# Kernel optimization log

Hardware: AMD Instinct MI355X
Metric: run time of the kernel (lower is better)

## Reference

```python
import jax, jax.numpy as jnp
import numpy as np

B, N_PTS, M_ROIS = 2, 8192, 2048
C_IN, O, H, NS = 128, 256, 4, 32
RADIUS = 1.6
BN_EPS = 1e-5
SCALE = 10.0  # point cloud extent


def setup_inputs() -> dict:
    key = jax.random.key(0)
    ks = jax.random.split(key, 20)
    f32 = jnp.float32
    Cg = C_IN + 3  # grouper concats relative xyz to features

    def kaiming(k, shape, fan_in):
        return jax.random.normal(k, shape, f32) * np.sqrt(2.0 / fan_in)

    inp = {
        "xyz": jax.random.uniform(ks[0], (B, N_PTS, 3), f32) * SCALE,
        "new_xyz": jax.random.uniform(ks[1], (B, M_ROIS, 3), f32) * SCALE,
        "features": jax.random.normal(ks[2], (B, C_IN, N_PTS), f32),
        # conv1d (kernel=1, no bias) weights, torch layout (out, in)
        "pos_w": kaiming(ks[3], (O, 3), 3),
        "key_w": kaiming(ks[4], (O, Cg), Cg),
        "val_w1": kaiming(ks[5], (O, Cg), Cg),
        "bn1_g": jnp.ones((O,), f32), "bn1_b": jnp.zeros((O,), f32),
        "val_w2": kaiming(ks[6], (O, O), O),
        "bn2_g": jnp.ones((O,), f32), "bn2_b": jnp.zeros((O,), f32),
        "attn_w": kaiming(ks[7], (H, O), O),
        # sigmoid-gated coefficient linears (no bias)
        "kc_w": kaiming(ks[8], (O, O), O),
        "qc_w": kaiming(ks[9], (O, O), O),
        "qkc_w": kaiming(ks[10], (O, O), O),
        "vc_w": kaiming(ks[11], (O, O), O),
        # cls/reg weight MLPs: Linear(O,O//2)+ReLU, Linear(O//2,1)+Sigmoid
        "cls_w1": kaiming(ks[12], (O // 2, O), O), "cls_b1": jnp.zeros((O // 2,), f32),
        "cls_w2": kaiming(ks[13], (1, O // 2), O // 2), "cls_b2": jnp.zeros((1,), f32),
        "reg_w1": kaiming(ks[14], (O // 2, O), O), "reg_b1": jnp.zeros((O // 2,), f32),
        "reg_w2": kaiming(ks[15], (1, O // 2), O // 2), "reg_b2": jnp.zeros((1,), f32),
    }
    return inp


def _bn(x, g, b):
    # eval-mode BatchNorm1d with running_mean=0, running_var=1 (init state)
    return g[None, :, None] * (x * (1.0 / np.sqrt(1.0 + BN_EPS))) + b[None, :, None]


def _conv1x1(w, x):  # (O,C) x (M,C,NS) -> (M,O,NS)
    return jnp.einsum('oc,mcn->mon', w, x)


def _ball_group(pts, q):
    # ball query: first NS points within RADIUS of each query (pad with first hit)
    n_tot = pts.shape[0]
    d2 = jnp.sum((q[:, None, :] - pts[None, :, :]) ** 2, axis=-1)  # (M, Ntot)
    order = jnp.where(d2 < RADIUS ** 2, jnp.arange(n_tot, dtype=jnp.int32), n_tot)
    neg_vals, idx = jax.lax.top_k(-order, NS)  # smallest indices among in-ball pts
    valid = (-neg_vals) < n_tot
    idx = jnp.where(valid, idx, idx[:, :1])  # pad with first neighbor
    has_any = valid[:, :1]
    idx = jnp.where(has_any, idx, 0)  # empty balls -> point 0
    return idx, ~has_any[:, 0]


def reference(xyz, new_xyz, features, pos_w, key_w, val_w1, bn1_g, bn1_b,
              val_w2, bn2_g, bn2_b, attn_w, kc_w, qc_w, qkc_w, vc_w,
              cls_w1, cls_b1, cls_w2, cls_b2, reg_w1, reg_b1, reg_w2, reg_b2):
    pts = xyz.reshape(-1, 3)                                   # (Ntot, 3)
    feats = features.transpose(0, 2, 1).reshape(-1, C_IN)      # (Ntot, C)
    q = new_xyz.reshape(-1, 3)                                 # (M, 3)

    idx, empty_mask = _ball_group(pts, q)                      # (M, NS)
    gx = pts[idx] - q[:, None, :]                              # relative xyz (M,NS,3)
    gxt = gx.transpose(0, 2, 1)                                # (M,3,NS)
    gf = jnp.concatenate([gx, feats[idx]], axis=-1).transpose(0, 2, 1)  # (M,C+3,NS)

    pos = jax.nn.relu(_conv1x1(pos_w, gxt))                    # (M,O,NS)
    key = jax.nn.relu(_conv1x1(key_w, gf))                     # (M,O,NS)
    v = jax.nn.relu(_bn(_conv1x1(val_w1, gf), bn1_g, bn1_b))
    val = jax.nn.relu(_bn(_conv1x1(val_w2, v), bn2_g, bn2_b))  # (M,O,NS)
    pos_key = pos * key

    sig = jax.nn.sigmoid
    v_c = sig(pos.mean(2) @ vc_w.T)                            # (M,O)
    q_c = sig(pos.mean(2) @ qc_w.T)
    k_c = sig(key.mean(2) @ kc_w.T)
    qk_c = sig(pos_key.mean(2) @ qkc_w.T)

    val = val + pos * v_c[:, :, None]
    attn_emb = pos * q_c[:, :, None] + key * k_c[:, :, None] + pos_key * qk_c[:, :, None]
    attn = jax.nn.softmax(jnp.einsum('ho,mon->mhn', attn_w, attn_emb), axis=-1)  # (M,H,NS)

    m = val.shape[0]
    vh = val.reshape(m, H, O // H, NS)
    new_features = jnp.einsum('mhdn,mhn->mhd', vh, attn).reshape(m, O)  # (M,O)

    def gate(x, w1, b1, w2, b2):
        return sig(jax.nn.relu(x @ w1.T + b1) @ w2.T + b2)

    cls_features = new_features * gate(new_features, cls_w1, cls_b1, cls_w2, cls_b2)
    reg_features = new_features * gate(new_features, reg_w1, reg_b1, reg_w2, reg_b2)
    return new_features, cls_features, reg_features
```

## Files before the change

### kernel.cpp

```cpp
#include <hip/hip_runtime.h>

#define DI __device__ __forceinline__

typedef __attribute__((ext_vector_type(8))) short bf16x8;
typedef __attribute__((ext_vector_type(4))) short s16x4;
typedef __attribute__((ext_vector_type(4))) float f32x4;

DI short f2bs(float x){ unsigned u = __float_as_uint(x);
  return (short)((u + 0x7FFF + ((u >> 16) & 1)) >> 16); }
DI float bs2f(short s){ return __uint_as_float(((unsigned)(unsigned short)s) << 16); }
DI f32x4 MFMA(bf16x8 a, bf16x8 b, f32x4 c){
  return __builtin_amdgcn_mfma_f32_16x16x32_bf16(a, b, c, 0, 0, 0);
}

constexpr int NP   = 8192;
constexpr int NTOT = 16384;
constexpr int M    = 4096;
constexpr int C    = 128;
constexpr int O    = 256;
constexpr int NS   = 32;
constexpr int H    = 4;
constexpr int KP   = 160;
constexpr int GFS  = 168;
constexpr int VS   = 264;
constexpr int NSP  = 34;
constexpr float BNS = 0.99999500003749969f;

__global__ __launch_bounds__(256) void k_prep(
    const float* __restrict__ feat,
    const float* __restrict__ kw, const float* __restrict__ v1w,
    const float* __restrict__ v2w,
    const float* __restrict__ vcw, const float* __restrict__ qcw,
    const float* __restrict__ kcw, const float* __restrict__ qkcw,
    const float* __restrict__ cw1, const float* __restrict__ rw1,
    const float* __restrict__ xyz, const float* __restrict__ nxyz,
    short* __restrict__ fT,
    short* __restrict__ keyP, short* __restrict__ v1P,
    short* __restrict__ v2b,
    short* __restrict__ gw,
    short* __restrict__ cw1b, short* __restrict__ rw1b,
    float* __restrict__ xyz4, float* __restrict__ nxyz4)
{
  __shared__ float tile[128][65];
  int blk = blockIdx.x;
  int t = threadIdx.x;
  if(blk < 256){
    int b  = blk >> 7;
    int n0 = (blk & 127) << 6;
    int nn = t & 63, c4 = t >> 6;
    const float* src = feat + (size_t)b * C * NP;
    for(int i = 0; i < 32; i++){
      int c = c4 * 32 + i;
      tile[c][nn] = src[(size_t)c * NP + n0 + nn];
    }
    __syncthreads();
    int c2 = t & 127, nb = t >> 7;
    for(int j = 0; j < 32; j++){
      int n = nb + j * 2;
      fT[((size_t)(b * NP + n0 + n)) * C + c2] = f2bs(tile[c2][n]);
    }
    return;
  }
  int i = (blk - 256) * 256 + t;
  if(i < O * KP){
    int o = i / KP, k = i % KP;
    float a = 0.0f, b = 0.0f;
    if(k < 128){ a = kw[o*131 + 3 + k]; b = v1w[o*131 + 3 + k]; }
    else if(k < 131){ a = kw[o*131 + (k - 128)]; b = v1w[o*131 + (k - 128)]; }
    keyP[i] = f2bs(a);
    v1P[i]  = f2bs(b);
  }
  if(i < O * O){
    v2b[i] = f2bs(v2w[i]);
    gw[0*O*O + i] = f2bs(vcw[i]);
    gw[1*O*O + i] = f2bs(qcw[i]);
    gw[2*O*O + i] = f2bs(kcw[i]);
    gw[3*O*O + i] = f2bs(qkcw[i]);
  }
  if(i < (O/2) * O){
    cw1b[i] = f2bs(cw1[i]);
    rw1b[i] = f2bs(rw1[i]);
  }
  if(i < NTOT){
    xyz4[i*4+0] = xyz[i*3+0];
    xyz4[i*4+1] = xyz[i*3+1];
    xyz4[i*4+2] = xyz[i*3+2];
    xyz4[i*4+3] = 0.0f;
  }
  if(i < M){
    nxyz4[i*4+0] = nxyz[i*3+0];
    nxyz4[i*4+1] = nxyz[i*3+1];
    nxyz4[i*4+2] = nxyz[i*3+2];
    nxyz4[i*4+3] = 0.0f;
  }
}

__global__ __launch_bounds__(256) void k_ballq(const float* __restrict__ xyz4,
                                               const float* __restrict__ nxyz4,
                                               int* __restrict__ idxo,
                                               float* __restrict__ gxo){
#pragma clang fp contract(off)
  int m = blockIdx.x;
  int t = threadIdx.x;
  int w = t >> 6, lane = t & 63;
  float qx = nxyz4[m*4+0], qy = nxyz4[m*4+1], qz = nxyz4[m*4+2];
  __shared__ int sel[NS];
  __shared__ int wcnt[2][4];
  int cnt = 0;
  int par = 0;
  for(int base = 0; base < NTOT; base += 256){
    int p = base + t;
    const float4 pt = *(const float4*)(xyz4 + (size_t)p*4);
    float dx = qx - pt.x, dy = qy - pt.y, dz = qz - pt.z;
    float d2 = dx*dx + dy*dy;
    d2 = d2 + dz*dz;
    bool pred = d2 < 2.56f;
    unsigned long long bal = __ballot(pred);
    if(lane == 0) wcnt[par][w] = __popcll(bal);
    __syncthreads();
    int c0 = wcnt[par][0], c1 = wcnt[par][1], c2 = wcnt[par][2], c3 = wcnt[par][3];
    int off = cnt + ((w > 0) ? c0 : 0) + ((w > 1) ? c1 : 0) + ((w > 2) ? c2 : 0);
    if(pred){
      int pos = off + __popcll(bal & ((1ull << lane) - 1ull));
      if(pos < NS) sel[pos] = p;
    }
    cnt += c0 + c1 + c2 + c3;
    par ^= 1;
    if(cnt >= NS) break;
  }
  __syncthreads();
  if(t < NS){
    int s = 0;
    if(cnt > 0) s = (t < cnt) ? sel[t] : sel[0];
    idxo[m*NS + t] = s;
    const float4 ps = *(const float4*)(xyz4 + (size_t)s*4);
    gxo[(m*NS+t)*3+0] = ps.x - qx;
    gxo[(m*NS+t)*3+1] = ps.y - qy;
    gxo[(m*NS+t)*3+2] = ps.z - qz;
  }
}

__global__ __launch_bounds__(256, 5) void k_conv(
    const short* __restrict__ fT,
    const short* __restrict__ keyP, const short* __restrict__ v1P,
    const short* __restrict__ v2b,
    const float* __restrict__ posw,
    const float* __restrict__ g1, const float* __restrict__ b1,
    const float* __restrict__ g2, const float* __restrict__ b2,
    const int* __restrict__ idxw, const float* __restrict__ gxw,
    short* __restrict__ keyT, short* __restrict__ valT,
    short* __restrict__ mPos, short* __restrict__ mKey, short* __restrict__ mPK,
    int q0)
{
  int lq = blockIdx.x, q = q0 + lq, t = threadIdx.x;
  int w = t >> 6, l = t & 63;
  int col = l & 15, kq = l >> 4;
  int ro = w * 64;
  __shared__ __align__(16) short gf[NS * GFS];
  __shared__ __align__(16) short buf[O * NSP];
  __shared__ float gxs[NS * 4];
  __shared__ int  sel[NS];
  if(t < NS){
    sel[t] = idxw[q*NS + t];
    gxs[t*4+0] = gxw[(q*NS+t)*3+0];
    gxs[t*4+1] = gxw[(q*NS+t)*3+1];
    gxs[t*4+2] = gxw[(q*NS+t)*3+2];
    gxs[t*4+3] = 0.0f;
  }
  __syncthreads();
  for(int i = 0; i < 2; i++){
    int n = w*8 + i*4 + kq;
    int p = sel[n];
    *(bf16x8*)&gf[n*GFS + col*8] = *(const bf16x8*)(fT + (size_t)p * C + col*8);
  }
  {
    int n = t & 31, kk = (t >> 5) * 4;
    for(int j = 0; j < 4; j++){
      int k = kk + j;
      float v = (k < 3) ? gxs[n*4 + k] : 0.0f;
      gf[n*GFS + 128 + k] = f2bs(v);
    }
  }
  __syncthreads();

  f32x4 acc[4][2];
  const f32x4 vzero = {0.0f, 0.0f, 0.0f, 0.0f};

  for(int mt=0;mt<4;mt++) for(int nt=0;nt<2;nt++) acc[mt][nt] = vzero;
  for(int ks = 0; ks < 5; ks++){
    bf16x8 b0 = *(const bf16x8*)&gf[col*GFS + ks*32 + kq*8];
    bf16x8 b1v = *(const bf16x8*)&gf[(16+col)*GFS + ks*32 + kq*8];
    for(int mt = 0; mt < 4; mt++){
      bf16x8 a = *(const bf16x8*)(keyP + (size_t)(ro + mt*16 + col)*KP + ks*32 + kq*8);
      acc[mt][0] = MFMA(a, b0, acc[mt][0]);
      acc[mt][1] = MFMA(a, b1v, acc[mt][1]);
    }
  }
  for(int mt=0;mt<4;mt++) for(int nt=0;nt<2;nt++)
    for(int r=0;r<4;r++){
      int o = ro + mt*16 + kq*4 + r;
      int n = nt*16 + col;
      buf[o*NSP + n] = f2bs(fmaxf(acc[mt][nt][r], 0.0f));
    }
  for(int mt=0;mt<4;mt++){
    for(int r=0;r<4;r++){
      int o = ro + mt*16 + kq*4 + r;
      float w0 = posw[o*3+0], w1 = posw[o*3+1], w2 = posw[o*3+2];
      float sp = 0, sk = 0, spk = 0;
      for(int nt=0;nt<2;nt++){
        int n = nt*16 + col;
        float p = fmaxf(w0*gxs[n*4+0] + w1*gxs[n*4+1] + w2*gxs[n*4+2], 0.0f);
        float v = fmaxf(acc[mt][nt][r], 0.0f);
        sp += p; sk += v; spk += p*v;
      }
      for(int msk=1; msk<16; msk<<=1){
        sp += __shfl_xor(sp, msk); sk += __shfl_xor(sk, msk); spk += __shfl_xor(spk, msk);
      }
      if(col == 0){
        mPos[lq*O+o] = f2bs(sp  * 0.03125f);
        mKey[lq*O+o] = f2bs(sk  * 0.03125f);
        mPK [lq*O+o] = f2bs(spk * 0.03125f);
      }
    }
  }
  __syncthreads();
  {
    uint vv[16];
    #pragma unroll
    for(int j=0;j<16;j++) vv[j] = *(const uint*)&buf[t*NSP + j*2];
    uint4* dst = (uint4*)(keyT + ((size_t)lq*O + t)*NS);
    dst[0] = make_uint4(vv[0],vv[1],vv[2],vv[3]);
    dst[1] = make_uint4(vv[4],vv[5],vv[6],vv[7]);
    dst[2] = make_uint4(vv[8],vv[9],vv[10],vv[11]);
    dst[3] = make_uint4(vv[12],vv[13],vv[14],vv[15]);
  }

  for(int mt=0;mt<4;mt++) for(int nt=0;nt<2;nt++) acc[mt][nt] = vzero;
  for(int ks = 0; ks < 5; ks++){
    bf16x8 b0 = *(const bf16x8*)&gf[col*GFS + ks*32 + kq*8];
    bf16x8 b1v = *(const bf16x8*)&gf[(16+col)*GFS + ks*32 + kq*8];
    for(int mt = 0; mt < 4; mt++){
      bf16x8 a = *(const bf16x8*)(v1P + (size_t)(ro + mt*16 + col)*KP + ks*32 + kq*8);
      acc[mt][0] = MFMA(a, b0, acc[mt][0]);
      acc[mt][1] = MFMA(a, b1v, acc[mt][1]);
    }
  }
  __syncthreads();
  for(int mt=0;mt<4;mt++){
    int o0 = ro + mt*16 + kq*4;
    float gg[4], bb[4];
    for(int r=0;r<4;r++){ gg[r] = g1[o0+r]; bb[r] = b1[o0+r]; }
    for(int nt=0;nt<2;nt++){
      s16x4 pk;
      for(int r=0;r<4;r++)
        pk[r] = f2bs(fmaxf(gg[r]*(acc[mt][nt][r] * BNS) + bb[r], 0.0f));
      int n = nt*16 + col;
      *(s16x4*)&buf[n*VS + o0] = pk;
    }
  }
  __syncthreads();

  for(int mt=0;mt<4;mt++) for(int nt=0;nt<2;nt++) acc[mt][nt] = vzero;
  for(int ks = 0; ks < 8; ks++){
    bf16x8 b0 = *(const bf16x8*)&buf[col*VS + ks*32 + kq*8];
    bf16x8 b1v = *(const bf16x8*)&buf[(16+col)*VS + ks*32 + kq*8];
    for(int mt = 0; mt < 4; mt++){
      bf16x8 a = *(const bf16x8*)(v2b + (size_t)(ro + mt*16 + col)*O + ks*32 + kq*8);
      acc[mt][0] = MFMA(a, b0, acc[mt][0]);
      acc[mt][1] = MFMA(a, b1v, acc[mt][1]);
    }
  }
  __syncthreads();
  for(int mt=0;mt<4;mt++){
    int o0 = ro + mt*16 + kq*4;
    float gg[4], bb[4];
    for(int r=0;r<4;r++){ gg[r] = g2[o0+r]; bb[r] = b2[o0+r]; }
    for(int nt=0;nt<2;nt++){
      int n = nt*16 + col;
      for(int r=0;r<4;r++)
        buf[(o0+r)*NSP + n] = f2bs(fmaxf(gg[r]*(acc[mt][nt][r] * BNS) + bb[r], 0.0f));
    }
  }
  __syncthreads();
  {
    uint vv[16];
    #pragma unroll
    for(int j=0;j<16;j++) vv[j] = *(const uint*)&buf[t*NSP + j*2];
    uint4* dst = (uint4*)(valT + ((size_t)lq*O + t)*NS);
    dst[0] = make_uint4(vv[0],vv[1],vv[2],vv[3]);
    dst[1] = make_uint4(vv[4],vv[5],vv[6],vv[7]);
    dst[2] = make_uint4(vv[8],vv[9],vv[10],vv[11]);
    dst[3] = make_uint4(vv[12],vv[13],vv[14],vv[15]);
  }
}

__global__ __launch_bounds__(256) void k_gates(
    const short* __restrict__ mPos, const short* __restrict__ mKey,
    const short* __restrict__ mPK, const short* __restrict__ gw,
    float* __restrict__ gates)
{
  int t = threadIdx.x, w = t >> 6, l = t & 63, col = l & 15, kq = l >> 4;
  int lq0 = blockIdx.x * 16;
  const short* A  = (w < 2) ? mPos : ((w == 2) ? mKey : mPK);
  const short* Wg = gw + (size_t)w * O * O;
  f32x4 acc[16];
  const f32x4 vzero = {0.0f,0.0f,0.0f,0.0f};
  for(int i=0;i<16;i++) acc[i] = vzero;
  for(int ks = 0; ks < 8; ks++){
    bf16x8 av = *(const bf16x8*)(A + (size_t)(lq0 + col)*O + ks*32 + kq*8);
    for(int nt = 0; nt < 16; nt++){
      bf16x8 bv = *(const bf16x8*)(Wg + (size_t)(nt*16 + col)*O + ks*32 + kq*8);
      acc[nt] = MFMA(av, bv, acc[nt]);
    }
  }
  for(int nt=0;nt<16;nt++) for(int r=0;r<4;r++){
    int lqq = lq0 + kq*4 + r;
    int oo = nt*16 + col;
    gates[((size_t)lqq*4 + w)*O + oo] = 1.0f / (1.0f + expf(-acc[nt][r]));
  }
}

__global__ __launch_bounds__(256) void k_attn(
    const short* __restrict__ keyT, const short* __restrict__ valT,
    const float* __restrict__ gxw, const float* __restrict__ posw,
    const float* __restrict__ attw, const float* __restrict__ gates,
    float* __restrict__ outNF, int q0)
{
  int lq = blockIdx.x, q = q0 + lq, t = threadIdx.x;
  __shared__ short embL[O * NSP];
  __shared__ float attnL[H * NS];
  __shared__ float gxs[NS * 3];
  __shared__ float partial[256];
  if(t < 96) gxs[t] = gxw[q*96 + t];
  float vc  = gates[((size_t)lq*4 + 0)*O + t];
  float qc  = gates[((size_t)lq*4 + 1)*O + t];
  float kc  = gates[((size_t)lq*4 + 2)*O + t];
  float qkc = gates[((size_t)lq*4 + 3)*O + t];
  float pw0 = posw[t*3+0], pw1 = posw[t*3+1], pw2 = posw[t*3+2];
  __syncthreads();
  float posr[NS];
  #pragma unroll
  for(int n = 0; n < NS; n++)
    posr[n] = fmaxf(pw0*gxs[n*3] + pw1*gxs[n*3+1] + pw2*gxs[n*3+2], 0.0f);
  {
    const short* kp = keyT + ((size_t)lq*O + t)*NS;
    #pragma unroll
    for(int g = 0; g < 4; g++){
      bf16x8 kg = *(const bf16x8*)(kp + g*8);
      #pragma unroll
      for(int jj = 0; jj < 4; jj++){
        int n0 = g*8 + jj*2;
        float kA = bs2f(kg[jj*2]),   kB = bs2f(kg[jj*2+1]);
        float eA = posr[n0]*qc   + kA*kc + posr[n0]*kA*qkc;
        float eB = posr[n0+1]*qc + kB*kc + posr[n0+1]*kB*qkc;
        unsigned pk = (unsigned)(unsigned short)f2bs(eA)
                    | ((unsigned)(unsigned short)f2bs(eB) << 16);
        *(unsigned*)&embL[t*NSP + n0] = pk;
      }
    }
  }
  __syncthreads();
  {
    int idx = t & 127, h = idx >> 5, n = idx & 31, half = t >> 7;
    const float* aw = attw + h*O + half*128;
    const short* eb = embL + (size_t)half*128*NSP + n;
    float s0=0, s1=0, s2=0, s3=0;
    for(int o = 0; o < 128; o += 4){
      s0 += aw[o+0] * bs2f(eb[(o+0)*NSP]);
      s1 += aw[o+1] * bs2f(eb[(o+1)*NSP]);
      s2 += aw[o+2] * bs2f(eb[(o+2)*NSP]);
      s3 += aw[o+3] * bs2f(eb[(o+3)*NSP]);
    }
    partial[t] = (s0 + s1) + (s2 + s3);
  }
  __syncthreads();
  if(t < 128){
    int h = t >> 5, n = t & 31;
    float s = partial[t] + partial[t + 128];
    float mx = s;
    for(int msk=1; msk<32; msk<<=1) mx = fmaxf(mx, __shfl_xor(mx, msk));
    float e = expf(s - mx);
    float sum = e;
    for(int msk=1; msk<32; msk<<=1) sum += __shfl_xor(sum, msk);
    attnL[h*NS + n] = e / sum;
  }
  __syncthreads();
  {
    const short* vp = valT + ((size_t)lq*O + t)*NS;
    int hh = t >> 6;
    float nf = 0;
    #pragma unroll
    for(int g = 0; g < 4; g++){
      bf16x8 vg = *(const bf16x8*)(vp + g*8);
      #pragma unroll
      for(int j = 0; j < 8; j++){
        int n = g*8 + j;
        nf += (bs2f(vg[j]) + posr[n]*vc) * attnL[hh*NS + n];
      }
    }
    outNF[(size_t)q*O + t] = nf;
  }
}

__global__ __launch_bounds__(256) void k_fgate(
    const float* __restrict__ nf,
    const short* __restrict__ cw1b, const float* __restrict__ cb1,
    const float* __restrict__ cw2, const float* __restrict__ cb2,
    const short* __restrict__ rw1b, const float* __restrict__ rb1,
    const float* __restrict__ rw2, const float* __restrict__ rb2,
    float* __restrict__ outC, float* __restrict__ outR)
{
  int t = threadIdx.x, w = t >> 6, l = t & 63, col = l & 15, kq = l >> 4;
  int q0 = blockIdx.x * 64;
  __shared__ float sC[64], sR[64];
  f32x4 acc[16];
  const f32x4 vzero = {0.0f,0.0f,0.0f,0.0f};
  for(int i=0;i<16;i++) acc[i] = vzero;
  int arow = q0 + w*16 + col;
  for(int ks = 0; ks < 8; ks++){
    union { bf16x8 v; short e[8]; } u;
    const float* ap = nf + (size_t)arow*O + ks*32 + kq*8;
    for(int j = 0; j < 8; j++) u.e[j] = f2bs(ap[j]);
    for(int nt = 0; nt < 16; nt++){
      const short* W1 = (nt < 8) ? cw1b : rw1b;
      int j = (nt & 7)*16 + col;
      bf16x8 bv = *(const bf16x8*)(W1 + (size_t)j*O + ks*32 + kq*8);
      acc[nt] = MFMA(u.v, bv, acc[nt]);
    }
  }
  for(int r = 0; r < 4; r++){
    float pc = 0, pr = 0;
    for(int nt = 0; nt < 8; nt++){
      int j = nt*16 + col;
      pc += fmaxf(acc[nt][r] + cb1[j], 0.0f) * cw2[j];
    }
    for(int nt = 8; nt < 16; nt++){
      int j = (nt - 8)*16 + col;
      pr += fmaxf(acc[nt][r] + rb1[j], 0.0f) * rw2[j];
    }
    for(int msk=1; msk<16; msk<<=1){ pc += __shfl_xor(pc, msk); pr += __shfl_xor(pr, msk); }
    if(col == 0){
      int qq = w*16 + kq*4 + r;
      sC[qq] = 1.0f / (1.0f + expf(-(pc + cb2[0])));
      sR[qq] = 1.0f / (1.0f + expf(-(pr + rb2[0])));
    }
  }
  __syncthreads();
  for(int it = 0; it < 16; it++){
    int qq = it*4 + w;
    float sc = sC[qq], sr = sR[qq];
    const f32x4 nv = *(const f32x4*)(nf + (size_t)(q0 + qq)*O + l*4);
    f32x4 oc, orr;
    #pragma unroll
    for(int r=0;r<4;r++){ oc[r] = nv[r]*sc; orr[r] = nv[r]*sr; }
    *(f32x4*)(outC + (size_t)(q0 + qq)*O + l*4) = oc;
    *(f32x4*)(outR + (size_t)(q0 + qq)*O + l*4) = orr;
  }
}

extern "C" void kernel_launch(void* const* d_in, const int* in_sizes, int n_in,
                              void* d_out, int out_size, void* d_ws, size_t ws_size,
                              hipStream_t stream)
{
  const float* xyz  = (const float*)d_in[0];
  const float* nxyz = (const float*)d_in[1];
  const float* feat = (const float*)d_in[2];
  const float* posw = (const float*)d_in[3];
  const float* keyw = (const float*)d_in[4];
  const float* v1w  = (const float*)d_in[5];
  const float* bn1g = (const float*)d_in[6];
  const float* bn1b = (const float*)d_in[7];
  const float* v2w  = (const float*)d_in[8];
  const float* bn2g = (const float*)d_in[9];
  const float* bn2b = (const float*)d_in[10];
  const float* attw = (const float*)d_in[11];
  const float* kcw  = (const float*)d_in[12];
  const float* qcw  = (const float*)d_in[13];
  const float* qkcw = (const float*)d_in[14];
  const float* vcw  = (const float*)d_in[15];
  const float* cw1  = (const float*)d_in[16];
  const float* cb1  = (const float*)d_in[17];
  const float* cw2  = (const float*)d_in[18];
  const float* cb2  = (const float*)d_in[19];
  const float* rw1  = (const float*)d_in[20];
  const float* rb1  = (const float*)d_in[21];
  const float* rw2  = (const float*)d_in[22];
  const float* rb2  = (const float*)d_in[23];

  const size_t fixedB = 12000000;
  const size_t perQ   = 40960;
  int Q = 64;
  for(int cand : {4096, 2048, 1024, 512, 256, 128}){
    if(fixedB + (size_t)cand*perQ <= ws_size){ Q = cand; break; }
  }

  char* p = (char*)d_ws;
  auto alloc = [&](size_t bytes){ char* r = p; p += (bytes + 255) & ~size_t(255); return r; };
  short* fT    = (short*)alloc((size_t)NTOT*C*2);
  short* keyP  = (short*)alloc((size_t)O*KP*2);
  short* v1P   = (short*)alloc((size_t)O*KP*2);
  short* v2b   = (short*)alloc((size_t)O*O*2);
  short* gw    = (short*)alloc((size_t)4*O*O*2);
  short* cw1b  = (short*)alloc((size_t)(O/2)*O*2);
  short* rw1b  = (short*)alloc((size_t)(O/2)*O*2);
  int*   idxw  = (int*)  alloc((size_t)M*NS*4);
  float* gxw   = (float*)alloc((size_t)M*NS*3*4);
  float* xyz4  = (float*)alloc((size_t)NTOT*4*4);
  float* nxyz4 = (float*)alloc((size_t)M*4*4);
  short* keyT  = (short*)alloc((size_t)Q*O*NS*2);
  short* valT  = (short*)alloc((size_t)Q*O*NS*2);
  short* mPos  = (short*)alloc((size_t)Q*O*2);
  short* mKey  = (short*)alloc((size_t)Q*O*2);
  short* mPK   = (short*)alloc((size_t)Q*O*2);
  float* gates = (float*)alloc((size_t)Q*4*O*4);

  float* outNF = (float*)d_out;
  float* outC  = outNF + (size_t)M*O;
  float* outR  = outC  + (size_t)M*O;

  k_prep     <<<512, 256, 0, stream>>>(feat, keyw, v1w, v2w, vcw, qcw, kcw, qkcw,
                                       cw1, rw1, xyz, nxyz,
                                       fT, keyP, v1P, v2b, gw, cw1b, rw1b, xyz4, nxyz4);
  k_ballq    <<<M,   256, 0, stream>>>(xyz4, nxyz4, idxw, gxw);
  for(int q0 = 0; q0 < M; q0 += Q){
    k_conv  <<<Q,    256, 0, stream>>>(fT, keyP, v1P, v2b,
                                       posw, bn1g, bn1b, bn2g, bn2b,
                                       idxw, gxw, keyT, valT, mPos, mKey, mPK, q0);
    k_gates <<<Q/16, 256, 0, stream>>>(mPos, mKey, mPK, gw, gates);
    k_attn  <<<Q,    256, 0, stream>>>(keyT, valT, gxw, posw, attw, gates, outNF, q0);
  }
  k_fgate   <<<M/64, 256, 0, stream>>>(outNF, cw1b, cb1, cw2, cb2, rw1b, rb1, rw2, rb2, outC, outR);
}
```

Measured before the change: 359.1 us.

## Fuse prep with ball query, fold final gating into attention, drop chunking

Ball query now runs as extra blocks of the prep kernel and reads the raw xyz arrays directly, so the padded xyz4 copies are gone. The final cls/reg gate MLP moves into the attention kernel as a per-query scalar dot-product reduction, which replaces the separate MFMA gate kernel and the re-read of new_features. The workspace-size-dependent chunk loop is removed and all intermediates are sized for the full M, cutting launches to four. This assumes the workspace always fits the full buffers. The fused gate computes per query in FP32 FMAs rather than with MFMA, and the ball query now reads unaligned 3-float points.

```diff
diff --git a/kernel.cpp b/kernel.cpp
--- a/kernel.cpp
+++ b/kernel.cpp
@@ -26,7 +26,7 @@
 constexpr int NSP  = 34;
 constexpr float BNS = 0.99999500003749969f;
 
-__global__ __launch_bounds__(256) void k_prep(
+__global__ __launch_bounds__(256) void k_front(
     const float* __restrict__ feat,
     const float* __restrict__ kw, const float* __restrict__ v1w,
     const float* __restrict__ v2w,
@@ -39,9 +39,10 @@
     short* __restrict__ v2b,
     short* __restrict__ gw,
     short* __restrict__ cw1b, short* __restrict__ rw1b,
-    float* __restrict__ xyz4, float* __restrict__ nxyz4)
+    int* __restrict__ idxo, float* __restrict__ gxo)
 {
-  __shared__ float tile[128][65];
+#pragma clang fp contract(off)
+  __shared__ __align__(16) float tile[128][65];
   int blk = blockIdx.x;
   int t = threadIdx.x;
   if(blk < 256){
@@ -61,64 +62,47 @@
     }
     return;
   }
-  int i = (blk - 256) * 256 + t;
-  if(i < O * KP){
-    int o = i / KP, k = i % KP;
-    float a = 0.0f, b = 0.0f;
-    if(k < 128){ a = kw[o*131 + 3 + k]; b = v1w[o*131 + 3 + k]; }
-    else if(k < 131){ a = kw[o*131 + (k - 128)]; b = v1w[o*131 + (k - 128)]; }
-    keyP[i] = f2bs(a);
-    v1P[i]  = f2bs(b);
-  }
-  if(i < O * O){
-    v2b[i] = f2bs(v2w[i]);
-    gw[0*O*O + i] = f2bs(vcw[i]);
-    gw[1*O*O + i] = f2bs(qcw[i]);
-    gw[2*O*O + i] = f2bs(kcw[i]);
-    gw[3*O*O + i] = f2bs(qkcw[i]);
-  }
-  if(i < (O/2) * O){
-    cw1b[i] = f2bs(cw1[i]);
-    rw1b[i] = f2bs(rw1[i]);
-  }
-  if(i < NTOT){
-    xyz4[i*4+0] = xyz[i*3+0];
-    xyz4[i*4+1] = xyz[i*3+1];
-    xyz4[i*4+2] = xyz[i*3+2];
-    xyz4[i*4+3] = 0.0f;
-  }
-  if(i < M){
-    nxyz4[i*4+0] = nxyz[i*3+0];
-    nxyz4[i*4+1] = nxyz[i*3+1];
-    nxyz4[i*4+2] = nxyz[i*3+2];
-    nxyz4[i*4+3] = 0.0f;
-  }
-}
-
-__global__ __launch_bounds__(256) void k_ballq(const float* __restrict__ xyz4,
-                                               const float* __restrict__ nxyz4,
-                                               int* __restrict__ idxo,
-                                               float* __restrict__ gxo){
-#pragma clang fp contract(off)
-  int m = blockIdx.x;
-  int t = threadIdx.x;
+  if(blk < 512){
+    int i = (blk - 256) * 256 + t;
+    if(i < O * KP){
+      int o = i / KP, k = i % KP;
+      float a = 0.0f, b = 0.0f;
+      if(k < 128){ a = kw[o*131 + 3 + k]; b = v1w[o*131 + 3 + k]; }
+      else if(k < 131){ a = kw[o*131 + (k - 128)]; b = v1w[o*131 + (k - 128)]; }
+      keyP[i] = f2bs(a);
+      v1P[i]  = f2bs(b);
+    }
+    if(i < O * O){
+      v2b[i] = f2bs(v2w[i]);
+      gw[0*O*O + i] = f2bs(vcw[i]);
+      gw[1*O*O + i] = f2bs(qcw[i]);
+      gw[2*O*O + i] = f2bs(kcw[i]);
+      gw[3*O*O + i] = f2bs(qkcw[i]);
+    }
+    if(i < (O/2) * O){
+      cw1b[i] = f2bs(cw1[i]);
+      rw1b[i] = f2bs(rw1[i]);
+    }
+    return;
+  }
+  int m = blk - 512;
   int w = t >> 6, lane = t & 63;
-  float qx = nxyz4[m*4+0], qy = nxyz4[m*4+1], qz = nxyz4[m*4+2];
-  __shared__ int sel[NS];
-  __shared__ int wcnt[2][4];
+  float qx = nxyz[m*3+0], qy = nxyz[m*3+1], qz = nxyz[m*3+2];
+  int* sel  = (int*)&tile[0][0];
+  int* wcnt = sel + NS;
   int cnt = 0;
   int par = 0;
   for(int base = 0; base < NTOT; base += 256){
     int p = base + t;
-    const float4 pt = *(const float4*)(xyz4 + (size_t)p*4);
-    float dx = qx - pt.x, dy = qy - pt.y, dz = qz - pt.z;
+    float px = xyz[p*3+0], py = xyz[p*3+1], pz = xyz[p*3+2];
+    float dx = qx - px, dy = qy - py, dz = qz - pz;
     float d2 = dx*dx + dy*dy;
     d2 = d2 + dz*dz;
     bool pred = d2 < 2.56f;
     unsigned long long bal = __ballot(pred);
-    if(lane == 0) wcnt[par][w] = __popcll(bal);
+    if(lane == 0) wcnt[par*4 + w] = __popcll(bal);
     __syncthreads();
-    int c0 = wcnt[par][0], c1 = wcnt[par][1], c2 = wcnt[par][2], c3 = wcnt[par][3];
+    int c0 = wcnt[par*4+0], c1 = wcnt[par*4+1], c2 = wcnt[par*4+2], c3 = wcnt[par*4+3];
     int off = cnt + ((w > 0) ? c0 : 0) + ((w > 1) ? c1 : 0) + ((w > 2) ? c2 : 0);
     if(pred){
       int pos = off + __popcll(bal & ((1ull << lane) - 1ull));
@@ -133,10 +117,9 @@
     int s = 0;
     if(cnt > 0) s = (t < cnt) ? sel[t] : sel[0];
     idxo[m*NS + t] = s;
-    const float4 ps = *(const float4*)(xyz4 + (size_t)s*4);
-    gxo[(m*NS+t)*3+0] = ps.x - qx;
-    gxo[(m*NS+t)*3+1] = ps.y - qy;
-    gxo[(m*NS+t)*3+2] = ps.z - qz;
+    gxo[(m*NS+t)*3+0] = xyz[s*3+0] - qx;
+    gxo[(m*NS+t)*3+1] = xyz[s*3+1] - qy;
+    gxo[(m*NS+t)*3+2] = xyz[s*3+2] - qz;
   }
 }
 
@@ -320,17 +303,24 @@
   }
 }
 
-__global__ __launch_bounds__(256) void k_attn(
+__global__ __launch_bounds__(256) void k_attnf(
     const short* __restrict__ keyT, const short* __restrict__ valT,
     const float* __restrict__ gxw, const float* __restrict__ posw,
     const float* __restrict__ attw, const float* __restrict__ gates,
-    float* __restrict__ outNF, int q0)
+    const short* __restrict__ cw1b, const float* __restrict__ cb1,
+    const float* __restrict__ cw2, const float* __restrict__ cb2,
+    const short* __restrict__ rw1b, const float* __restrict__ rb1,
+    const float* __restrict__ rw2, const float* __restrict__ rb2,
+    float* __restrict__ outNF, float* __restrict__ outC, float* __restrict__ outR,
+    int q0)
 {
   int lq = blockIdx.x, q = q0 + lq, t = threadIdx.x;
   __shared__ short embL[O * NSP];
   __shared__ float attnL[H * NS];
   __shared__ float gxs[NS * 3];
   __shared__ float partial[256];
+  __shared__ float sGate[2];
+  float* nfL = (float*)embL;
   if(t < 96) gxs[t] = gxw[q*96 + t];
   float vc  = gates[((size_t)lq*4 + 0)*O + t];
   float qc  = gates[((size_t)lq*4 + 1)*O + t];
@@ -385,6 +375,7 @@
     attnL[h*NS + n] = e / sum;
   }
   __syncthreads();
+  float nft;
   {
     const short* vp = valT + ((size_t)lq*O + t)*NS;
     int hh = t >> 6;
@@ -398,64 +389,39 @@
         nf += (bs2f(vg[j]) + posr[n]*vc) * attnL[hh*NS + n];
       }
     }
-    outNF[(size_t)q*O + t] = nf;
-  }
-}
-
-__global__ __launch_bounds__(256) void k_fgate(
-    const float* __restrict__ nf,
-    const short* __restrict__ cw1b, const float* __restrict__ cb1,
-    const float* __restrict__ cw2, const float* __restrict__ cb2,
-    const short* __restrict__ rw1b, const float* __restrict__ rb1,
-    const float* __restrict__ rw2, const float* __restrict__ rb2,
-    float* __restrict__ outC, float* __restrict__ outR)
-{
-  int t = threadIdx.x, w = t >> 6, l = t & 63, col = l & 15, kq = l >> 4;
-  int q0 = blockIdx.x * 64;
-  __shared__ float sC[64], sR[64];
-  f32x4 acc[16];
-  const f32x4 vzero = {0.0f,0.0f,0.0f,0.0f};
-  for(int i=0;i<16;i++) acc[i] = vzero;
-  int arow = q0 + w*16 + col;
-  for(int ks = 0; ks < 8; ks++){
-    union { bf16x8 v; short e[8]; } u;
-    const float* ap = nf + (size_t)arow*O + ks*32 + kq*8;
-    for(int j = 0; j < 8; j++) u.e[j] = f2bs(ap[j]);
-    for(int nt = 0; nt < 16; nt++){
-      const short* W1 = (nt < 8) ? cw1b : rw1b;
-      int j = (nt & 7)*16 + col;
-      bf16x8 bv = *(const bf16x8*)(W1 + (size_t)j*O + ks*32 + kq*8);
-      acc[nt] = MFMA(u.v, bv, acc[nt]);
-    }
-  }
-  for(int r = 0; r < 4; r++){
-    float pc = 0, pr = 0;
-    for(int nt = 0; nt < 8; nt++){
-      int j = nt*16 + col;
-      pc += fmaxf(acc[nt][r] + cb1[j], 0.0f) * cw2[j];
-    }
-    for(int nt = 8; nt < 16; nt++){
-      int j = (nt - 8)*16 + col;
-      pr += fmaxf(acc[nt][r] + rb1[j], 0.0f) * rw2[j];
-    }
-    for(int msk=1; msk<16; msk<<=1){ pc += __shfl_xor(pc, msk); pr += __shfl_xor(pr, msk); }
-    if(col == 0){
-      int qq = w*16 + kq*4 + r;
-      sC[qq] = 1.0f / (1.0f + expf(-(pc + cb2[0])));
-      sR[qq] = 1.0f / (1.0f + expf(-(pr + rb2[0])));
-    }
-  }
-  __syncthreads();
-  for(int it = 0; it < 16; it++){
-    int qq = it*4 + w;
-    float sc = sC[qq], sr = sR[qq];
-    const f32x4 nv = *(const f32x4*)(nf + (size_t)(q0 + qq)*O + l*4);
-    f32x4 oc, orr;
-    #pragma unroll
-    for(int r=0;r<4;r++){ oc[r] = nv[r]*sc; orr[r] = nv[r]*sr; }
-    *(f32x4*)(outC + (size_t)(q0 + qq)*O + l*4) = oc;
-    *(f32x4*)(outR + (size_t)(q0 + qq)*O + l*4) = orr;
-  }
+    nft = nf;
+    outNF[(size_t)q*O + t] = nft;
+  }
+  __syncthreads();
+  nfL[t] = nft;
+  __syncthreads();
+  {
+    int j = t & 127;
+    const short* W1 = (t < 128) ? cw1b : rw1b;
+    float bias = (t < 128) ? cb1[j] : rb1[j];
+    float w2v  = (t < 128) ? cw2[j] : rw2[j];
+    const short* row = W1 + (size_t)j * O;
+    float h = 0;
+    for(int c8 = 0; c8 < 32; c8++){
+      bf16x8 wv = *(const bf16x8*)(row + c8*8);
+      #pragma unroll
+      for(int e = 0; e < 8; e++) h += bs2f(wv[e]) * nfL[c8*8 + e];
+    }
+    partial[t] = fmaxf(h + bias, 0.0f) * w2v;
+  }
+  __syncthreads();
+  if(t < 64){
+    float s = partial[t] + partial[t + 64];
+    for(int msk=1; msk<64; msk<<=1) s += __shfl_xor(s, msk);
+    if(t == 0) sGate[0] = 1.0f / (1.0f + expf(-(s + cb2[0])));
+  } else if(t >= 128 && t < 192){
+    float s = partial[t] + partial[t + 64];
+    for(int msk=1; msk<64; msk<<=1) s += __shfl_xor(s, msk);
+    if(t == 128) sGate[1] = 1.0f / (1.0f + expf(-(s + rb2[0])));
+  }
+  __syncthreads();
+  outC[(size_t)q*O + t] = nft * sGate[0];
+  outR[(size_t)q*O + t] = nft * sGate[1];
 }
 
 extern "C" void kernel_launch(void* const* d_in, const int* in_sizes, int n_in,
@@ -487,13 +453,6 @@
   const float* rw2  = (const float*)d_in[22];
   const float* rb2  = (const float*)d_in[23];
 
-  const size_t fixedB = 12000000;
-  const size_t perQ   = 40960;
-  int Q = 64;
-  for(int cand : {4096, 2048, 1024, 512, 256, 128}){
-    if(fixedB + (size_t)cand*perQ <= ws_size){ Q = cand; break; }
-  }
-
   char* p = (char*)d_ws;
   auto alloc = [&](size_t bytes){ char* r = p; p += (bytes + 255) & ~size_t(255); return r; };
   short* fT    = (short*)alloc((size_t)NTOT*C*2);
@@ -505,29 +464,25 @@
   short* rw1b  = (short*)alloc((size_t)(O/2)*O*2);
   int*   idxw  = (int*)  alloc((size_t)M*NS*4);
   float* gxw   = (float*)alloc((size_t)M*NS*3*4);
-  float* xyz4  = (float*)alloc((size_t)NTOT*4*4);
-  float* nxyz4 = (float*)alloc((size_t)M*4*4);
-  short* keyT  = (short*)alloc((size_t)Q*O*NS*2);
-  short* valT  = (short*)alloc((size_t)Q*O*NS*2);
-  short* mPos  = (short*)alloc((size_t)Q*O*2);
-  short* mKey  = (short*)alloc((size_t)Q*O*2);
-  short* mPK   = (short*)alloc((size_t)Q*O*2);
-  float* gates = (float*)alloc((size_t)Q*4*O*4);
+  short* keyT  = (short*)alloc((size_t)M*O*NS*2);
+  short* valT  = (short*)alloc((size_t)M*O*NS*2);
+  short* mPos  = (short*)alloc((size_t)M*O*2);
+  short* mKey  = (short*)alloc((size_t)M*O*2);
+  short* mPK   = (short*)alloc((size_t)M*O*2);
+  float* gates = (float*)alloc((size_t)M*4*O*4);
 
   float* outNF = (float*)d_out;
   float* outC  = outNF + (size_t)M*O;
   float* outR  = outC  + (size_t)M*O;
 
-  k_prep     <<<512, 256, 0, stream>>>(feat, keyw, v1w, v2w, vcw, qcw, kcw, qkcw,
-                                       cw1, rw1, xyz, nxyz,
-                                       fT, keyP, v1P, v2b, gw, cw1b, rw1b, xyz4, nxyz4);
-  k_ballq    <<<M,   256, 0, stream>>>(xyz4, nxyz4, idxw, gxw);
-  for(int q0 = 0; q0 < M; q0 += Q){
-    k_conv  <<<Q,    256, 0, stream>>>(fT, keyP, v1P, v2b,
-                                       posw, bn1g, bn1b, bn2g, bn2b,
-                                       idxw, gxw, keyT, valT, mPos, mKey, mPK, q0);
-    k_gates <<<Q/16, 256, 0, stream>>>(mPos, mKey, mPK, gw, gates);
-    k_attn  <<<Q,    256, 0, stream>>>(keyT, valT, gxw, posw, attw, gates, outNF, q0);
-  }
-  k_fgate   <<<M/64, 256, 0, stream>>>(outNF, cw1b, cb1, cw2, cb2, rw1b, rb1, rw2, rb2, outC, outR);
-}
+  k_front <<<512 + M, 256, 0, stream>>>(feat, keyw, v1w, v2w, vcw, qcw, kcw, qkcw,
+                                        cw1, rw1, xyz, nxyz,
+                                        fT, keyP, v1P, v2b, gw, cw1b, rw1b, idxw, gxw);
+  k_conv  <<<M,    256, 0, stream>>>(fT, keyP, v1P, v2b,
+                                     posw, bn1g, bn1b, bn2g, bn2b,
+                                     idxw, gxw, keyT, valT, mPos, mKey, mPK, 0);
+  k_gates <<<M/16, 256, 0, stream>>>(mPos, mKey, mPK, gw, gates);
+  k_attnf <<<M,    256, 0, stream>>>(keyT, valT, gxw, posw, attw, gates,
+                                     cw1b, cb1, cw2, cb2, rw1b, rb1, rw2, rb2,
+                                     outNF, outC, outR, 0);
+}
```

Result: slower. 410.9 us (+14.4%).
